# Kernel optimization log

Measured on AMD Instinct MI355X. Metric: run time of the kernel, lower is better.

Reference implementation:

```python
import jax, jax.numpy as jnp
import numpy as np

D = 20          # embedding dim (hardcoded in original module)
N_REL = 200     # relation vocab size (table has N_REL+1 rows)
N_TIME = 365    # time embedding table size
L = 3           # propagation layers
E = 2_000_000   # edges per layer
N = 1_000_000   # node-slot pool per layer
B = 64          # batch size
N_ENT = 1_000_003


def setup_inputs() -> dict:
    key = jax.random.key(0)
    ks = jax.random.split(key, 16)
    src_idx = jax.random.randint(ks[0], (L, E), 0, N, dtype=jnp.int32)
    dst_idx = jax.random.randint(ks[1], (L, E), 0, N, dtype=jnp.int32)
    rel_idx = jax.random.randint(ks[2], (L, E), 0, N_REL + 1, dtype=jnp.int32)
    qrel_idx = jax.random.randint(ks[3], (L, E), 0, N_REL + 1, dtype=jnp.int32)
    # signed relative time (edge_time - query_time); abs() must stay < N_TIME
    rel_time = jax.random.randint(ks[4], (L, E), -(N_TIME - 1), N_TIME, dtype=jnp.int32)
    node_batch = jax.random.randint(ks[5], (N,), 0, B, dtype=jnp.int32)
    node_ent = jnp.arange(N, dtype=jnp.int32)  # unique entity per final node slot
    s = 0.1
    rela_embed = jax.random.normal(ks[6], (N_REL + 1, D), jnp.float32) * s
    time_embed = jax.random.normal(ks[7], (N_TIME, D), jnp.float32) * s
    w_att1 = jax.random.normal(ks[8], (30, 3 * D), jnp.float32) * s
    w_att2 = jax.random.normal(ks[9], (1, 30), jnp.float32) * s
    w_past = jax.random.normal(ks[10], (D, D), jnp.float32) * s
    w_now = jax.random.normal(ks[11], (D, D), jnp.float32) * s
    w_future = jax.random.normal(ks[12], (D, D), jnp.float32) * s
    w_cls = jax.random.normal(ks[13], (D,), jnp.float32) * s
    b_cls = jnp.zeros((), jnp.float32)
    return dict(src_idx=src_idx, dst_idx=dst_idx, rel_idx=rel_idx,
                qrel_idx=qrel_idx, rel_time=rel_time, node_batch=node_batch,
                node_ent=node_ent, rela_embed=rela_embed, time_embed=time_embed,
                w_att1=w_att1, w_att2=w_att2, w_past=w_past, w_now=w_now,
                w_future=w_future, w_cls=w_cls, b_cls=b_cls,
                batch_size=B, n_ent=N_ENT)


def reference(src_idx, dst_idx, rel_idx, qrel_idx, rel_time, node_batch,
              node_ent, rela_embed, time_embed, w_att1, w_att2, w_past,
              w_now, w_future, w_cls, b_cls, batch_size, n_ent):
    n_layers = src_idx.shape[0]
    n_nodes = node_batch.shape[0]
    d = rela_embed.shape[1]
    hidden = jnp.zeros((n_nodes, d), dtype=rela_embed.dtype)
    for l in range(n_layers):
        rt = rel_time[l]                         # [E] signed relative time
        h_src = hidden[src_idx[l]]               # [E, D] gather
        r_emb = rela_embed[rel_idx[l]]           # [E, D]
        t_emb = time_embed[jnp.abs(rt)]          # [E, D]
        embed_rel = h_src + r_emb + t_emb
        # conditional time-branch MLP (mask-partitioned linear, same math as
        # the original's boolean-masked assignments)
        fut = embed_rel @ w_future.T
        now = embed_rel @ w_now.T
        pst = embed_rel @ w_past.T
        transformed = jnp.where((rt > 0)[:, None], fut,
                       jnp.where((rt == 0)[:, None], now, pst))
        # attention over concat(hidden_src, rel_emb, query_rel_emb)  [E, 3D]
        att_in = jnp.concatenate([h_src, r_emb, rela_embed[qrel_idx[l]]], axis=1)
        score = jax.nn.sigmoid(jax.nn.relu(att_in @ w_att1.T) @ w_att2.T)  # [E,1]
        msg = score * transformed                # [E, D]
        hidden = jax.ops.segment_sum(msg, dst_idx[l], num_segments=n_nodes)
        hidden = jax.nn.leaky_relu(hidden)       # default slope 0.01, as torch
    result = hidden @ w_cls + b_cls              # [N]
    score_all = jnp.zeros((batch_size, n_ent), dtype=result.dtype)
    score_all = score_all.at[node_batch, node_ent].set(result)
    return score_all
```

## Files before the change

### kernel.cpp

```cpp
#include <hip/hip_runtime.h>
#include <hip/hip_bf16.h>
#include <cstdint>

#define DD 20
#define HID 30
#define NB_SCAN 1024
#define MROW 21

__device__ __forceinline__ void load20(const float* __restrict__ p, float* r){
  const float4* q = (const float4*)p;
#pragma unroll
  for (int i=0;i<5;i++){ float4 v=q[i]; r[4*i+0]=v.x; r[4*i+1]=v.y; r[4*i+2]=v.z; r[4*i+3]=v.w; }
}

__global__ void k_prep(const float* __restrict__ rela, const float* __restrict__ w1,
                       const float* __restrict__ wp, const float* __restrict__ wn,
                       const float* __restrict__ wf,
                       float* __restrict__ W3, float* __restrict__ AR, float* __restrict__ AQ,
                       int nrel){
  int t = blockIdx.x*blockDim.x + threadIdx.x;
  if (t < 3*DD*DD){
    int s = t/(DD*DD), idx = t%(DD*DD);
    W3[t] = (s==0)?wp[idx]:((s==1)?wn[idx]:wf[idx]);
  }
  if (t < nrel*HID){
    int r=t/HID, j=t-r*HID;
    float sr=0.f, sq=0.f;
#pragma unroll
    for (int k=0;k<DD;k++){
      float e = rela[r*DD+k];
      sr += e*w1[j*3*DD + DD + k];
      sq += e*w1[j*3*DD + 2*DD + k];
    }
    AR[r*32+j]=sr; AQ[r*32+j]=sq;
  }
}

__global__ void k_rt(const float* __restrict__ rela, const float* __restrict__ timee,
                     const float* __restrict__ W3, float* __restrict__ RT,
                     int nrel, int ntime){
  int row = blockIdx.x*blockDim.x+threadIdx.x;
  int tot = 3*nrel*ntime;
  if (row>=tot) return;
  int per = nrel*ntime;
  int sel = row/per; int rem = row - sel*per; int r = rem/ntime; int t = rem - r*ntime;
  float e[DD], tv[DD];
  load20(rela + (size_t)r*DD, e);
  load20(timee + (size_t)t*DD, tv);
#pragma unroll
  for (int k=0;k<DD;k++) e[k]+=tv[k];
  const float* W = W3 + sel*DD*DD;
  float o[DD];
#pragma unroll
  for (int i=0;i<DD;i++){
    const float4* wr = (const float4*)(W + i*DD);
    float s=0.f;
#pragma unroll
    for (int c=0;c<5;c++){ float4 w=wr[c]; s += e[4*c]*w.x + e[4*c+1]*w.y + e[4*c+2]*w.z + e[4*c+3]*w.w; }
    o[i]=s;
  }
  float4* op=(float4*)(RT + (size_t)row*DD);
#pragma unroll
  for (int c=0;c<5;c++){ float4 v; v.x=o[4*c]; v.y=o[4*c+1]; v.z=o[4*c+2]; v.w=o[4*c+3]; op[c]=v; }
}

__global__ void k_hist_all(const int* __restrict__ dst, int* __restrict__ cnt,
                           int* __restrict__ rank, int LE, int E, int N){
  int e = blockIdx.x*blockDim.x+threadIdx.x;
  if (e>=LE) return;
  int l = e/E;
  int d = dst[e];
  rank[e] = atomicAdd(&cnt[(size_t)l*N+d], 1);
}

__global__ void k_scan_part(const int* __restrict__ cnt, int* __restrict__ part, int M, int C){
  __shared__ int sm[256];
  int b=blockIdx.x, t=threadIdx.x;
  int lo=b*C, hi=lo+C; if (hi>M) hi=M; if (lo>M) lo=M;
  int s=0;
  for (int i=lo+t; i<hi; i+=256) s+=cnt[i];
  sm[t]=s; __syncthreads();
  for (int o=128;o>0;o>>=1){ if (t<o) sm[t]+=sm[t+o]; __syncthreads(); }
  if (t==0) part[b]=sm[0];
}

__global__ void k_scan_top(int* __restrict__ part){
  __shared__ int sm[NB_SCAN];
  int t=threadIdx.x;
  int v=part[t]; sm[t]=v; __syncthreads();
  for (int o=1;o<NB_SCAN;o<<=1){
    int u=(t>=o)?sm[t-o]:0; __syncthreads();
    sm[t]+=u; __syncthreads();
  }
  part[t]=sm[t]-v;
}

__global__ void k_scan_write(const int* __restrict__ cnt, const int* __restrict__ part,
                             int* __restrict__ rowptr, int M, int C){
  __shared__ int sm[256];
  int b=blockIdx.x, t=threadIdx.x;
  int lo=b*C, hi=lo+C; if (hi>M) hi=M; if (lo>M) lo=M;
  int run=part[b];
  for (int base=lo; base<hi; base+=256){
    int i=base+t;
    int v=(i<hi)?cnt[i]:0;
    sm[t]=v; __syncthreads();
    for (int o=1;o<256;o<<=1){
      int u=(t>=o)?sm[t-o]:0; __syncthreads();
      sm[t]+=u; __syncthreads();
    }
    if (i<hi) rowptr[i]=run+sm[t]-v;
    int tot=sm[255];
    __syncthreads();
    run+=tot;
  }
  if (hi==M && t==0) rowptr[M]=run;
}

__global__ void k_scat_all(const int* __restrict__ src, const int* __restrict__ dst,
                           const int* __restrict__ rel, const int* __restrict__ qrel,
                           const int* __restrict__ rtm,
                           const int* __restrict__ rank, const int* __restrict__ rowptr,
                           int4* __restrict__ recs, int LE, int E, int N){
  int e = blockIdx.x*blockDim.x+threadIdx.x;
  if (e>=LE) return;
  int l = e/E;
  int d = dst[e];
  int pos = rowptr[(size_t)l*N+d] + rank[e];
  recs[pos] = make_int4(src[e], rel[e] | (qrel[e]<<16), rtm[e], d);
}

template<bool HASH>
__global__ void __launch_bounds__(256) k_layer(
    const int4* __restrict__ recs,
    const float* __restrict__ hin, float* __restrict__ hout,
    const float* __restrict__ RT, const float* __restrict__ AR, const float* __restrict__ AQ,
    const float* __restrict__ w1, const float* __restrict__ w2, const float* __restrict__ W3,
    int E, int nrel, int ntime)
{
  __shared__ float sW1h[HID*DD];
  __shared__ float sW2[32];
  __shared__ float sW3[3*DD*DD];
  __shared__ float smsg[256*MROW];
  __shared__ int   sdst[256];
  __shared__ int   s_prevdst, s_nextdst;
  if (HASH){
    for (int t=threadIdx.x; t<HID*DD; t+=blockDim.x){ int j=t/DD,k=t-j*DD; sW1h[t]=w1[j*3*DD+k]; }
    for (int t=threadIdx.x; t<3*DD*DD; t+=blockDim.x) sW3[t]=W3[t];
  }
  if (threadIdx.x<HID) sW2[threadIdx.x]=w2[threadIdx.x];

  int tid = threadIdx.x;
  int bstart = blockIdx.x*256;
  int bsize = E - bstart; if (bsize>256) bsize=256;
  int j = bstart + tid;
  bool active = (tid < bsize);

  if (tid==0){
    s_prevdst = (bstart>0) ? recs[-1 + (ptrdiff_t)bstart].w : -1;
    s_nextdst = (bstart+bsize < E) ? recs[bstart+bsize].w : -1;
  }

  int dstv = -1;
  float m[DD];
  if (active){
    int4 rc = recs[j];
    int s = rc.x;
    int r = rc.y & 0xFFFF;
    int q = ((unsigned)rc.y) >> 16;
    int t = rc.z;
    dstv  = rc.w;
    int sel = (t>0)?2:((t==0)?1:0);
    int ta = (t<0)?-t:t;

    float h[DD];
    if (HASH){
      load20(hin+(size_t)s*DD, h);
#pragma unroll
      for (int i=0;i<DD;i++) h[i]=fmaxf(h[i],0.01f*h[i]);
    }

    float a[HID];
    {
      const float4* ap=(const float4*)(AR+(size_t)r*32);
      const float4* qp=(const float4*)(AQ+(size_t)q*32);
#pragma unroll
      for (int c=0;c<7;c++){
        float4 x=ap[c], y=qp[c];
        a[4*c+0]=x.x+y.x; a[4*c+1]=x.y+y.y; a[4*c+2]=x.z+y.z; a[4*c+3]=x.w+y.w;
      }
      float2 x=*(const float2*)(AR+(size_t)r*32+28);
      float2 y=*(const float2*)(AQ+(size_t)q*32+28);
      a[28]=x.x+y.x; a[29]=x.y+y.y;
    }
    if (HASH){
#pragma unroll
      for (int jj=0;jj<HID;jj++){
        const float4* wr=(const float4*)&sW1h[jj*DD];
        float sum=a[jj];
#pragma unroll
        for (int c=0;c<5;c++){ float4 w=wr[c]; sum += h[4*c]*w.x+h[4*c+1]*w.y+h[4*c+2]*w.z+h[4*c+3]*w.w; }
        a[jj]=sum;
      }
    }
    float z=0.f;
#pragma unroll
    for (int jj=0;jj<HID;jj++) z += fmaxf(a[jj],0.f)*sW2[jj];
    float score = 1.f/(1.f+__expf(-z));

    float tr[DD];
    load20(RT + ((size_t)(sel*nrel+r)*ntime + ta)*DD, tr);
    if (HASH){
      const float* Ws = sW3 + sel*DD*DD;
#pragma unroll
      for (int i=0;i<DD;i++){
        const float4* wr=(const float4*)(Ws+i*DD);
        float sum=tr[i];
#pragma unroll
        for (int c=0;c<5;c++){ float4 w=wr[c]; sum += h[4*c]*w.x+h[4*c+1]*w.y+h[4*c+2]*w.z+h[4*c+3]*w.w; }
        tr[i]=sum;
      }
    }
#pragma unroll
    for (int i=0;i<DD;i++){ m[i]=score*tr[i]; smsg[tid*MROW+i]=m[i]; }
  }
  sdst[tid] = active ? dstv : -2;
  __syncthreads();

  if (active){
    bool isHead = (tid==0) ? (s_prevdst != dstv) : (sdst[tid-1] != dstv);
    if (isHead || tid==0){
      int k=tid+1;
      for (; k<bsize && sdst[k]==dstv; ++k){
        const float* row=&smsg[k*MROW];
#pragma unroll
        for (int i=0;i<DD;i++) m[i]+=row[i];
      }
      bool crossStart = (tid==0 && !isHead);
      bool crossEnd   = (k==bsize) && (s_nextdst==dstv);
      float* o = hout + (size_t)dstv*DD;
      if (crossStart || crossEnd){
#pragma unroll
        for (int i=0;i<DD;i++) atomicAdd(o+i, m[i]);
      } else {
        float4* op=(float4*)o;
#pragma unroll
        for (int c=0;c<5;c++){ float4 v; v.x=m[4*c]; v.y=m[4*c+1]; v.z=m[4*c+2]; v.w=m[4*c+3]; op[c]=v; }
      }
    }
  }
}

__global__ void k_final(const float* __restrict__ h, const float* __restrict__ wcls,
                        const float* __restrict__ bcls, const int* __restrict__ nb,
                        const int* __restrict__ ne, const int* __restrict__ nentp,
                        float* __restrict__ out, int N){
  int n = blockIdx.x*blockDim.x+threadIdx.x;
  if (n>=N) return;
  float acc = bcls[0];
  const float4* q=(const float4*)(h+(size_t)n*DD);
#pragma unroll
  for (int c=0;c<5;c++){
    float4 v=q[c];
    float x0=fmaxf(v.x,0.01f*v.x), x1=fmaxf(v.y,0.01f*v.y);
    float x2=fmaxf(v.z,0.01f*v.z), x3=fmaxf(v.w,0.01f*v.w);
    acc += x0*wcls[4*c]+x1*wcls[4*c+1]+x2*wcls[4*c+2]+x3*wcls[4*c+3];
  }
  long long stride = nentp[0];
  out[(long long)nb[n]*stride + ne[n]] = acc;
}

template<bool HASH>
__global__ void __launch_bounds__(256) k_edge(
    const int* __restrict__ src, const int* __restrict__ dst,
    const int* __restrict__ rel, const int* __restrict__ qrel,
    const int* __restrict__ rtm,
    const float* __restrict__ hin, float* __restrict__ hout,
    const float* __restrict__ RT, const float* __restrict__ AR, const float* __restrict__ AQ,
    const float* __restrict__ w1, const float* __restrict__ w2, const float* __restrict__ W3,
    int E, int nrel, int ntime)
{
  __shared__ float sW1h[HID*DD];
  __shared__ float sW2[32];
  __shared__ float sW3[3*DD*DD];
  for (int t=threadIdx.x; t<HID*DD; t+=blockDim.x){ int j=t/DD,k=t-j*DD; sW1h[t]=w1[j*3*DD+k]; }
  if (threadIdx.x<HID) sW2[threadIdx.x]=w2[threadIdx.x];
  for (int t=threadIdx.x; t<3*DD*DD; t+=blockDim.x) sW3[t]=W3[t];
  __syncthreads();
  int e = blockIdx.x*blockDim.x+threadIdx.x;
  if (e>=E) return;
  int s=src[e], d=dst[e], r=rel[e], q=qrel[e], t=rtm[e];
  int sel = (t>0)?2:((t==0)?1:0);
  int ta = (t<0)?-t:t;
  float h[DD];
  if (HASH){
    load20(hin+(size_t)s*DD, h);
#pragma unroll
    for (int i=0;i<DD;i++) h[i]=fmaxf(h[i],0.01f*h[i]);
  }
  float a[HID];
  {
    const float4* ap=(const float4*)(AR+(size_t)r*32);
    const float4* qp=(const float4*)(AQ+(size_t)q*32);
#pragma unroll
    for (int c=0;c<7;c++){
      float4 x=ap[c], y=qp[c];
      a[4*c+0]=x.x+y.x; a[4*c+1]=x.y+y.y; a[4*c+2]=x.z+y.z; a[4*c+3]=x.w+y.w;
    }
    float2 x=*(const float2*)(AR+(size_t)r*32+28);
    float2 y=*(const float2*)(AQ+(size_t)q*32+28);
    a[28]=x.x+y.x; a[29]=x.y+y.y;
  }
  if (HASH){
#pragma unroll
    for (int j=0;j<HID;j++){
      const float4* wr=(const float4*)&sW1h[j*DD];
      float sum=a[j];
#pragma unroll
      for (int c=0;c<5;c++){ float4 w=wr[c]; sum += h[4*c]*w.x+h[4*c+1]*w.y+h[4*c+2]*w.z+h[4*c+3]*w.w; }
      a[j]=sum;
    }
  }
  float z=0.f;
#pragma unroll
  for (int j=0;j<HID;j++) z += fmaxf(a[j],0.f)*sW2[j];
  float score = 1.f/(1.f+__expf(-z));
  float tr[DD];
  load20(RT + ((size_t)(sel*nrel+r)*ntime + ta)*DD, tr);
  if (HASH){
    const float* Ws = sW3 + sel*DD*DD;
#pragma unroll
    for (int i=0;i<DD;i++){
      const float4* wr=(const float4*)(Ws+i*DD);
      float sum=tr[i];
#pragma unroll
      for (int c=0;c<5;c++){ float4 w=wr[c]; sum += h[4*c]*w.x+h[4*c+1]*w.y+h[4*c+2]*w.z+h[4*c+3]*w.w; }
      tr[i]=sum;
    }
  }
  float* o = hout + (size_t)d*DD;
#pragma unroll
  for (int i=0;i<DD;i++) atomicAdd(o+i, score*tr[i]);
}

__global__ void k_result(const float* __restrict__ h, const float* __restrict__ wcls,
                         const float* __restrict__ bcls, float* __restrict__ res, int N){
  int i = blockIdx.x*blockDim.x+threadIdx.x;
  if (i>=N) return;
  float acc = bcls[0];
  const float4* q=(const float4*)(h+(size_t)i*DD);
#pragma unroll
  for (int c=0;c<5;c++){
    float4 v=q[c];
    float x0=fmaxf(v.x,0.01f*v.x), x1=fmaxf(v.y,0.01f*v.y);
    float x2=fmaxf(v.z,0.01f*v.z), x3=fmaxf(v.w,0.01f*v.w);
    acc += x0*wcls[4*c]+x1*wcls[4*c+1]+x2*wcls[4*c+2]+x3*wcls[4*c+3];
  }
  res[i]=acc;
}

__global__ void k_scatter(const float* __restrict__ res, const int* __restrict__ nb,
                          const int* __restrict__ ne, const int* __restrict__ nentp,
                          float* __restrict__ out, int N){
  int i=blockIdx.x*blockDim.x+threadIdx.x;
  if (i>=N) return;
  long long stride = nentp[0];
  out[(long long)nb[i]*stride + ne[i]] = res[i];
}

extern "C" void kernel_launch(void* const* d_in, const int* in_sizes, int n_in,
                              void* d_out, int out_size, void* d_ws, size_t ws_size,
                              hipStream_t stream){
  const int*   src =(const int*)d_in[0];
  const int*   dst =(const int*)d_in[1];
  const int*   rel =(const int*)d_in[2];
  const int*   qrel=(const int*)d_in[3];
  const int*   rtm =(const int*)d_in[4];
  const int*   nb  =(const int*)d_in[5];
  const int*   ne  =(const int*)d_in[6];
  const float* rela=(const float*)d_in[7];
  const float* timee=(const float*)d_in[8];
  const float* w1  =(const float*)d_in[9];
  const float* w2  =(const float*)d_in[10];
  const float* wp  =(const float*)d_in[11];
  const float* wn  =(const float*)d_in[12];
  const float* wf  =(const float*)d_in[13];
  const float* wcls=(const float*)d_in[14];
  const float* bcls=(const float*)d_in[15];
  const int*   nentp=(const int*)d_in[17];

  const int Lc=3;
  int LE=in_sizes[0]; int E=LE/Lc;
  int N=in_sizes[5];
  int nrel=in_sizes[7]/DD;
  int ntime=in_sizes[8]/DD;
  int M = Lc*N;

  auto al=[](size_t x){ return (x+(size_t)255)&~(size_t)255; };
  size_t szBuf =al((size_t)N*DD*4);
  size_t szRT  =al((size_t)3*nrel*ntime*DD*4);
  size_t szA   =al((size_t)nrel*32*4);
  size_t szW3  =al((size_t)3*DD*DD*4);
  size_t szRow =al(((size_t)M+1)*4);
  size_t szRank=al((size_t)LE*4);
  size_t szCnt =al((size_t)M*4);
  size_t szRecs=al((size_t)LE*16);
  size_t szPart=al((size_t)NB_SCAN*4);
  size_t need = 2*szBuf+szRT+2*szA+szW3+szRow+szRank+szCnt+szRecs+szPart;

  dim3 blk(256);
  int prepTot = (3*DD*DD > nrel*HID) ? 3*DD*DD : nrel*HID;
  int rtTot=3*nrel*ntime;

  if (ws_size >= need){
    char* base=(char*)d_ws;
    size_t off=0;
    float* buf0=(float*)(base+off); off+=szBuf;
    float* buf1=(float*)(base+off); off+=szBuf;
    float* RT  =(float*)(base+off); off+=szRT;
    float* AR  =(float*)(base+off); off+=szA;
    float* AQ  =(float*)(base+off); off+=szA;
    float* W3  =(float*)(base+off); off+=szW3;
    int*   rowptr=(int*)(base+off); off+=szRow;
    int*   rank=(int*)(base+off);  off+=szRank;
    int*   cnt =(int*)(base+off);  off+=szCnt;
    int4*  recs=(int4*)(base+off); off+=szRecs;
    int*   part=(int*)(base+off);  off+=szPart;

    k_prep<<<dim3((prepTot+255)/256),blk,0,stream>>>(rela,w1,wp,wn,wf,W3,AR,AQ,nrel);
    k_rt<<<dim3((rtTot+255)/256),blk,0,stream>>>(rela,timee,W3,RT,nrel,ntime);

    (void)hipMemsetAsync(cnt,0,(size_t)M*4,stream);
    k_hist_all<<<dim3((LE+255)/256),blk,0,stream>>>(dst,cnt,rank,LE,E,N);
    int C=(M+NB_SCAN-1)/NB_SCAN;
    k_scan_part<<<dim3(NB_SCAN),blk,0,stream>>>(cnt,part,M,C);
    k_scan_top<<<dim3(1),dim3(NB_SCAN),0,stream>>>(part);
    k_scan_write<<<dim3(NB_SCAN),blk,0,stream>>>(cnt,part,rowptr,M,C);
    k_scat_all<<<dim3((LE+255)/256),blk,0,stream>>>(src,dst,rel,qrel,rtm,rank,rowptr,recs,LE,E,N);

    (void)hipMemsetAsync(d_out,0,(size_t)out_size*sizeof(float),stream);
    (void)hipMemsetAsync(buf0,0,(size_t)N*DD*4,stream);
    (void)hipMemsetAsync(buf1,0,(size_t)N*DD*4,stream);

    dim3 egrid((E+255)/256);
    dim3 ngrid((N+255)/256);
    k_layer<false><<<egrid,blk,0,stream>>>(recs,nullptr,buf0,RT,AR,AQ,w1,w2,W3,E,nrel,ntime);
    k_layer<true><<<egrid,blk,0,stream>>>(recs+(size_t)E,buf0,buf1,RT,AR,AQ,w1,w2,W3,E,nrel,ntime);
    (void)hipMemsetAsync(buf0,0,(size_t)N*DD*4,stream);
    k_layer<true><<<egrid,blk,0,stream>>>(recs+(size_t)2*E,buf1,buf0,RT,AR,AQ,w1,w2,W3,E,nrel,ntime);

    k_final<<<ngrid,blk,0,stream>>>(buf0,wcls,bcls,nb,ne,nentp,(float*)d_out,N);
  } else {
    char* base=(char*)d_out; float* res=(float*)d_ws;
    size_t off=0;
    float* buf0=(float*)(base+off); off+=szBuf;
    float* buf1=(float*)(base+off); off+=szBuf;
    float* RT  =(float*)(base+off); off+=szRT;
    float* AR  =(float*)(base+off); off+=szA;
    float* AQ  =(float*)(base+off); off+=szA;
    float* W3  =(float*)(base+off); off+=szW3;
    k_prep<<<dim3((prepTot+255)/256),blk,0,stream>>>(rela,w1,wp,wn,wf,W3,AR,AQ,nrel);
    k_rt<<<dim3((rtTot+255)/256),blk,0,stream>>>(rela,timee,W3,RT,nrel,ntime);
    dim3 egrid((E+255)/256);
    dim3 ngrid((N+255)/256);
    (void)hipMemsetAsync(buf0,0,(size_t)N*DD*4,stream);
    k_edge<false><<<egrid,blk,0,stream>>>(src,dst,rel,qrel,rtm,nullptr,buf0,RT,AR,AQ,w1,w2,W3,E,nrel,ntime);
    (void)hipMemsetAsync(buf1,0,(size_t)N*DD*4,stream);
    k_edge<true><<<egrid,blk,0,stream>>>(src+(size_t)E,dst+(size_t)E,rel+(size_t)E,qrel+(size_t)E,rtm+(size_t)E,
                                         buf0,buf1,RT,AR,AQ,w1,w2,W3,E,nrel,ntime);
    (void)hipMemsetAsync(buf0,0,(size_t)N*DD*4,stream);
    k_edge<true><<<egrid,blk,0,stream>>>(src+(size_t)2*E,dst+(size_t)2*E,rel+(size_t)2*E,qrel+(size_t)2*E,rtm+(size_t)2*E,
                                         buf1,buf0,RT,AR,AQ,w1,w2,W3,E,nrel,ntime);
    k_result<<<ngrid,blk,0,stream>>>(buf0,wcls,bcls,res,N);
    (void)hipMemsetAsync(d_out,0,(size_t)out_size*sizeof(float),stream);
    k_scatter<<<ngrid,blk,0,stream>>>(res,nb,ne,nentp,(float*)d_out,N);
  }
}
```

Baseline: 1.149 ms.

## Fuse per-layer histogram, zeroing and final classifier into layer kernels

Restructures the workspace path so each layer's CSR build runs per layer, with the next layer's histogram atomics folded into the current layer kernel's grid as extra blocks. Output and buffer zeroing are merged into a single pre-kernel, and the last layer computes the classifier score directly for segments that do not cross a block boundary. Cross-boundary segments are collected into a list and finished by a small sparse kernel. This removes the separate final pass over all nodes and several memsets, at the cost of more launches (per-layer scans), a fixed-size boundary list (8192 entries), and bias-only writes for empty nodes.

Result: faster. 1.122 ms (-2.4%).

```diff
diff --git a/kernel.cpp b/kernel.cpp
--- a/kernel.cpp
+++ b/kernel.cpp
@@ -64,13 +64,22 @@
   for (int c=0;c<5;c++){ float4 v; v.x=o[4*c]; v.y=o[4*c+1]; v.z=o[4*c+2]; v.w=o[4*c+3]; op[c]=v; }
 }
 
-__global__ void k_hist_all(const int* __restrict__ dst, int* __restrict__ cnt,
-                           int* __restrict__ rank, int LE, int E, int N){
-  int e = blockIdx.x*blockDim.x+threadIdx.x;
-  if (e>=LE) return;
-  int l = e/E;
-  int d = dst[e];
-  rank[e] = atomicAdd(&cnt[(size_t)l*N+d], 1);
+__global__ void __launch_bounds__(256) k_pre(const int* __restrict__ dst0, int* __restrict__ cnt0,
+        int* __restrict__ rank0, int E,
+        float4* __restrict__ dout4, size_t nd4,
+        float4* __restrict__ b04, float4* __restrict__ b14, size_t nb4){
+  int g=blockIdx.x, tid=threadIdx.x;
+  int half=gridDim.x>>1;
+  if (g & 1){
+    int stride=half*256;
+    for (int e=(g>>1)*256+tid; e<E; e+=stride)
+      rank0[e]=atomicAdd(&cnt0[dst0[e]],1);
+  } else {
+    float4 z=make_float4(0.f,0.f,0.f,0.f);
+    size_t i=(size_t)(g>>1)*256+tid, st=(size_t)half*256;
+    for (size_t k=i;k<nd4;k+=st) dout4[k]=z;
+    for (size_t k=i;k<nb4;k+=st){ b04[k]=z; b14[k]=z; }
+  }
 }
 
 __global__ void k_scan_part(const int* __restrict__ cnt, int* __restrict__ part, int M, int C){
@@ -117,27 +126,60 @@
   if (hi==M && t==0) rowptr[M]=run;
 }
 
-__global__ void k_scat_all(const int* __restrict__ src, const int* __restrict__ dst,
-                           const int* __restrict__ rel, const int* __restrict__ qrel,
-                           const int* __restrict__ rtm,
-                           const int* __restrict__ rank, const int* __restrict__ rowptr,
-                           int4* __restrict__ recs, int LE, int E, int N){
-  int e = blockIdx.x*blockDim.x+threadIdx.x;
-  if (e>=LE) return;
-  int l = e/E;
-  int d = dst[e];
-  int pos = rowptr[(size_t)l*N+d] + rank[e];
-  recs[pos] = make_int4(src[e], rel[e] | (qrel[e]<<16), rtm[e], d);
-}
-
-template<bool HASH>
-__global__ void __launch_bounds__(256) k_layer(
+__global__ void __launch_bounds__(256) k_scat(const int* __restrict__ src,const int* __restrict__ dst,
+  const int* __restrict__ rel,const int* __restrict__ qrel,const int* __restrict__ rtm,
+  const int* __restrict__ rank,const int* __restrict__ rowptr,int4* __restrict__ recs,int E,
+  int xb,int mode,
+  float* __restrict__ dout,const int* __restrict__ nb,const int* __restrict__ ne,
+  const int* __restrict__ nentp,const float* __restrict__ bcls,int N,
+  float4* __restrict__ zbuf,size_t nz4,int* __restrict__ listc){
+  int g=blockIdx.x, tid=threadIdx.x;
+  if (g<xb){
+    if (mode==0){
+      float b=bcls[0]; long long stride=nentp[0];
+      for (int n=g*256+tid;n<N;n+=xb*256) dout[(long long)nb[n]*stride+ne[n]]=b;
+    } else {
+      if (g==0&&tid==0) *listc=0;
+      float4 z=make_float4(0.f,0.f,0.f,0.f);
+      for (size_t k=(size_t)g*256+tid;k<nz4;k+=(size_t)xb*256) zbuf[k]=z;
+    }
+    return;
+  }
+  int e=(g-xb)*256+tid;
+  if (e>=E) return;
+  int d=dst[e];
+  int pos=rowptr[d]+rank[e];
+  recs[pos]=make_int4(src[e], rel[e]|(qrel[e]<<16), rtm[e], d);
+}
+
+template<bool HASH,bool HIST,bool FINAL>
+__global__ void __launch_bounds__(256) k_fused(
     const int4* __restrict__ recs,
     const float* __restrict__ hin, float* __restrict__ hout,
     const float* __restrict__ RT, const float* __restrict__ AR, const float* __restrict__ AQ,
     const float* __restrict__ w1, const float* __restrict__ w2, const float* __restrict__ W3,
-    int E, int nrel, int ntime)
+    int E, int nrel, int ntime,
+    const int* __restrict__ ndst, int* __restrict__ ncnt, int* __restrict__ nrank, int nE,
+    const float* __restrict__ wcls, const float* __restrict__ bcls,
+    const int* __restrict__ nbv, const int* __restrict__ nev, const int* __restrict__ nentp,
+    float* __restrict__ outp, int* __restrict__ list, int* __restrict__ listc)
 {
+  int lb;
+  if (HIST){
+    int g=blockIdx.x;
+    int r=g%3, b3=g/3;
+    if (r==2){
+      int H=gridDim.x/3;
+      int stride=H*256;
+      for (int e=b3*256+threadIdx.x; e<nE; e+=stride)
+        nrank[e]=atomicAdd(&ncnt[ndst[e]],1);
+      return;
+    }
+    lb=b3*2+r;
+  } else lb=blockIdx.x;
+  int bstart=lb*256;
+  if (bstart>=E) return;
+
   __shared__ float sW1h[HID*DD];
   __shared__ float sW2[32];
   __shared__ float sW3[3*DD*DD];
@@ -151,7 +193,6 @@
   if (threadIdx.x<HID) sW2[threadIdx.x]=w2[threadIdx.x];
 
   int tid = threadIdx.x;
-  int bstart = blockIdx.x*256;
   int bsize = E - bstart; if (bsize>256) bsize=256;
   int j = bstart + tid;
   bool active = (tid < bsize);
@@ -160,6 +201,7 @@
     s_prevdst = (bstart>0) ? recs[-1 + (ptrdiff_t)bstart].w : -1;
     s_nextdst = (bstart+bsize < E) ? recs[bstart+bsize].w : -1;
   }
+  __syncthreads();
 
   int dstv = -1;
   float m[DD];
@@ -227,47 +269,54 @@
   sdst[tid] = active ? dstv : -2;
   __syncthreads();
 
-  if (active){
-    bool isHead = (tid==0) ? (s_prevdst != dstv) : (sdst[tid-1] != dstv);
-    if (isHead || tid==0){
-      int k=tid+1;
-      for (; k<bsize && sdst[k]==dstv; ++k){
-        const float* row=&smsg[k*MROW];
-#pragma unroll
-        for (int i=0;i<DD;i++) m[i]+=row[i];
-      }
-      bool crossStart = (tid==0 && !isHead);
-      bool crossEnd   = (k==bsize) && (s_nextdst==dstv);
-      float* o = hout + (size_t)dstv*DD;
-      if (crossStart || crossEnd){
-#pragma unroll
-        for (int i=0;i<DD;i++) atomicAdd(o+i, m[i]);
-      } else {
-        float4* op=(float4*)o;
-#pragma unroll
-        for (int c=0;c<5;c++){ float4 v; v.x=m[4*c]; v.y=m[4*c+1]; v.z=m[4*c+2]; v.w=m[4*c+3]; op[c]=v; }
-      }
-    }
-  }
-}
-
-__global__ void k_final(const float* __restrict__ h, const float* __restrict__ wcls,
-                        const float* __restrict__ bcls, const int* __restrict__ nb,
-                        const int* __restrict__ ne, const int* __restrict__ nentp,
-                        float* __restrict__ out, int N){
-  int n = blockIdx.x*blockDim.x+threadIdx.x;
-  if (n>=N) return;
-  float acc = bcls[0];
-  const float4* q=(const float4*)(h+(size_t)n*DD);
-#pragma unroll
-  for (int c=0;c<5;c++){
-    float4 v=q[c];
-    float x0=fmaxf(v.x,0.01f*v.x), x1=fmaxf(v.y,0.01f*v.y);
-    float x2=fmaxf(v.z,0.01f*v.z), x3=fmaxf(v.w,0.01f*v.w);
-    acc += x0*wcls[4*c]+x1*wcls[4*c+1]+x2*wcls[4*c+2]+x3*wcls[4*c+3];
-  }
-  long long stride = nentp[0];
-  out[(long long)nb[n]*stride + ne[n]] = acc;
+  if (!active) return;
+  bool isHead = (tid==0) ? (s_prevdst != dstv) : (sdst[tid-1] != dstv);
+  if (!(isHead || tid==0)) return;
+  int k=tid+1;
+  for (; k<bsize && sdst[k]==dstv; ++k){
+    const float* row=&smsg[k*MROW];
+#pragma unroll
+    for (int i=0;i<DD;i++) m[i]+=row[i];
+  }
+  bool crossStart = (tid==0 && !isHead);
+  bool crossEnd   = (k==bsize) && (s_nextdst==dstv);
+  if (crossStart || crossEnd){
+    float* o = hout + (size_t)dstv*DD;
+#pragma unroll
+    for (int i=0;i<DD;i++) atomicAdd(o+i, m[i]);
+    if (FINAL && isHead){
+      int p = atomicAdd(listc,1);
+      list[p] = dstv;
+    }
+  } else {
+    if (!FINAL){
+      float4* op=(float4*)(hout + (size_t)dstv*DD);
+#pragma unroll
+      for (int c=0;c<5;c++){ float4 v; v.x=m[4*c]; v.y=m[4*c+1]; v.z=m[4*c+2]; v.w=m[4*c+3]; op[c]=v; }
+    } else {
+      float rsum=bcls[0];
+#pragma unroll
+      for (int i=0;i<DD;i++){ float x=fmaxf(m[i],0.01f*m[i]); rsum += x*wcls[i]; }
+      long long stride = nentp[0];
+      outp[(long long)nbv[dstv]*stride + nev[dstv]] = rsum;
+    }
+  }
+}
+
+__global__ void __launch_bounds__(256) k_fsparse(const float* __restrict__ buf,
+   const float* __restrict__ wcls,const float* __restrict__ bcls,
+   const int* __restrict__ nb,const int* __restrict__ ne,const int* __restrict__ nentp,
+   float* __restrict__ out,const int* __restrict__ list,const int* __restrict__ listc){
+  int c=*listc;
+  int i=blockIdx.x*blockDim.x+threadIdx.x;
+  if (i>=c) return;
+  int n=list[i];
+  float rsum=bcls[0];
+  const float* h=buf+(size_t)n*DD;
+#pragma unroll
+  for (int jj=0;jj<DD;jj++){ float v=h[jj]; float x=fmaxf(v,0.01f*v); rsum+=x*wcls[jj]; }
+  long long stride=nentp[0];
+  out[(long long)nb[n]*stride+ne[n]]=rsum;
 }
 
 template<bool HASH>
@@ -394,19 +443,19 @@
   int N=in_sizes[5];
   int nrel=in_sizes[7]/DD;
   int ntime=in_sizes[8]/DD;
-  int M = Lc*N;
 
   auto al=[](size_t x){ return (x+(size_t)255)&~(size_t)255; };
   size_t szBuf =al((size_t)N*DD*4);
   size_t szRT  =al((size_t)3*nrel*ntime*DD*4);
   size_t szA   =al((size_t)nrel*32*4);
   size_t szW3  =al((size_t)3*DD*DD*4);
-  size_t szRow =al(((size_t)M+1)*4);
+  size_t szRow =al((size_t)Lc*((size_t)N+1)*4);
   size_t szRank=al((size_t)LE*4);
-  size_t szCnt =al((size_t)M*4);
+  size_t szCnt =al((size_t)Lc*N*4);
   size_t szRecs=al((size_t)LE*16);
   size_t szPart=al((size_t)NB_SCAN*4);
-  size_t need = 2*szBuf+szRT+2*szA+szW3+szRow+szRank+szCnt+szRecs+szPart;
+  size_t szList=al((size_t)(8192+16)*4);
+  size_t need = 2*szBuf+szRT+2*szA+szW3+szRow+szRank+szCnt+szRecs+szPart+szList;
 
   dim3 blk(256);
   int prepTot = (3*DD*DD > nrel*HID) ? 3*DD*DD : nrel*HID;
@@ -426,30 +475,53 @@
     int*   cnt =(int*)(base+off);  off+=szCnt;
     int4*  recs=(int4*)(base+off); off+=szRecs;
     int*   part=(int*)(base+off);  off+=szPart;
-
+    int*   listc=(int*)(base+off);
+    int*   list =listc+16;          off+=szList;
+
+    float* dout=(float*)d_out;
+
+    (void)hipMemsetAsync(cnt,0,(size_t)Lc*N*4,stream);
     k_prep<<<dim3((prepTot+255)/256),blk,0,stream>>>(rela,w1,wp,wn,wf,W3,AR,AQ,nrel);
     k_rt<<<dim3((rtTot+255)/256),blk,0,stream>>>(rela,timee,W3,RT,nrel,ntime);
 
-    (void)hipMemsetAsync(cnt,0,(size_t)M*4,stream);
-    k_hist_all<<<dim3((LE+255)/256),blk,0,stream>>>(dst,cnt,rank,LE,E,N);
-    int C=(M+NB_SCAN-1)/NB_SCAN;
-    k_scan_part<<<dim3(NB_SCAN),blk,0,stream>>>(cnt,part,M,C);
-    k_scan_top<<<dim3(1),dim3(NB_SCAN),0,stream>>>(part);
-    k_scan_write<<<dim3(NB_SCAN),blk,0,stream>>>(cnt,part,rowptr,M,C);
-    k_scat_all<<<dim3((LE+255)/256),blk,0,stream>>>(src,dst,rel,qrel,rtm,rank,rowptr,recs,LE,E,N);
-
-    (void)hipMemsetAsync(d_out,0,(size_t)out_size*sizeof(float),stream);
-    (void)hipMemsetAsync(buf0,0,(size_t)N*DD*4,stream);
-    (void)hipMemsetAsync(buf1,0,(size_t)N*DD*4,stream);
-
-    dim3 egrid((E+255)/256);
-    dim3 ngrid((N+255)/256);
-    k_layer<false><<<egrid,blk,0,stream>>>(recs,nullptr,buf0,RT,AR,AQ,w1,w2,W3,E,nrel,ntime);
-    k_layer<true><<<egrid,blk,0,stream>>>(recs+(size_t)E,buf0,buf1,RT,AR,AQ,w1,w2,W3,E,nrel,ntime);
-    (void)hipMemsetAsync(buf0,0,(size_t)N*DD*4,stream);
-    k_layer<true><<<egrid,blk,0,stream>>>(recs+(size_t)2*E,buf1,buf0,RT,AR,AQ,w1,w2,W3,E,nrel,ntime);
-
-    k_final<<<ngrid,blk,0,stream>>>(buf0,wcls,bcls,nb,ne,nentp,(float*)d_out,N);
+    size_t nd4=(size_t)out_size>>2;
+    size_t nb4=(size_t)N*DD/4;
+    k_pre<<<dim3(8192),blk,0,stream>>>(dst,cnt,rank,E,(float4*)dout,nd4,(float4*)buf0,(float4*)buf1,nb4);
+
+    int C=(N+NB_SCAN-1)/NB_SCAN;
+    int LB=(E+255)/256;
+    int H=(LB+1)/2;
+
+    for (int l=0;l<Lc;++l){
+      int* cnt_l = cnt + (size_t)l*N;
+      int* row_l = rowptr + (size_t)l*(N+1);
+      k_scan_part<<<dim3(NB_SCAN),blk,0,stream>>>(cnt_l,part,N,C);
+      k_scan_top<<<dim3(1),dim3(NB_SCAN),0,stream>>>(part);
+      k_scan_write<<<dim3(NB_SCAN),blk,0,stream>>>(cnt_l,part,row_l,N,C);
+      size_t eo=(size_t)l*E;
+      int xb = (l==0)?1024:((l==2)?2048:0);
+      int mode=(l==0)?0:2;
+      k_scat<<<dim3(xb+LB),blk,0,stream>>>(src+eo,dst+eo,rel+eo,qrel+eo,rtm+eo,
+          rank+eo,row_l,recs+eo,E,xb,mode,
+          dout,nb,ne,nentp,bcls,N,(float4*)buf0,nb4,listc);
+      if (l==0){
+        k_fused<false,true,false><<<dim3(3*H),blk,0,stream>>>(recs,nullptr,buf0,
+            RT,AR,AQ,w1,w2,W3,E,nrel,ntime,
+            dst+(size_t)E,cnt+(size_t)N,rank+(size_t)E,E,
+            nullptr,nullptr,nullptr,nullptr,nullptr,nullptr,nullptr,nullptr);
+      } else if (l==1){
+        k_fused<true,true,false><<<dim3(3*H),blk,0,stream>>>(recs+(size_t)E,buf0,buf1,
+            RT,AR,AQ,w1,w2,W3,E,nrel,ntime,
+            dst+(size_t)2*E,cnt+(size_t)2*N,rank+(size_t)2*E,E,
+            nullptr,nullptr,nullptr,nullptr,nullptr,nullptr,nullptr,nullptr);
+      } else {
+        k_fused<true,false,true><<<dim3(LB),blk,0,stream>>>(recs+(size_t)2*E,buf1,buf0,
+            RT,AR,AQ,w1,w2,W3,E,nrel,ntime,
+            nullptr,nullptr,nullptr,0,
+            wcls,bcls,nb,ne,nentp,dout,list,listc);
+      }
+    }
+    k_fsparse<<<dim3(32),blk,0,stream>>>(buf0,wcls,bcls,nb,ne,nentp,dout,list,listc);
   } else {
     char* base=(char*)d_out; float* res=(float*)d_ws;
     size_t off=0;
```
